# Kernel tuning notes

Hardware: AMD Instinct MI355X
Metric: run time of the kernel (lower is better)

## Reference

```python
import jax, jax.numpy as jnp
import numpy as np

# static config (matches init_kwargs)
P = 16          # proj_patch_dim (window size)
F = 128         # fmap_dim
NH = F // P     # windows per side = 8
N = P * P       # tokens per window = 256
H = 8           # attn_heads
A = 32          # attn_dim (head dim)
C = 32          # leff_filters_out (channels)
INNER = 128     # leff_filters
B = 8           # batch
EPS = 1e-5

# relative-position index (static)
_c = np.stack(np.meshgrid(np.arange(P), np.arange(P), indexing='ij'))  # [2,P,P]
_f = _c.reshape(2, -1)                                                  # [2,N]
_r = _f[:, :, None] - _f[:, None, :]                                    # [2,N,N]
_rpi = (_r[0] + P - 1) * (2 * P - 1) + (_r[1] + P - 1)                  # [N,N]
RPI = jnp.asarray(_rpi.reshape(-1))

# shifted-window attention mask (static)
_sm = np.zeros((F, F), np.float32)
_cnt = 0
_slices = (slice(0, -P), slice(-P, -P // 2), slice(-P // 2, None))
for _hs in _slices:
    for _ws in _slices:
        _sm[_hs, _ws] = _cnt
        _cnt += 1
_smw = _sm.reshape(NH, P, NH, P).transpose(0, 2, 1, 3).reshape(NH * NH, N)
_am = _smw[:, None, :] - _smw[:, :, None]
_am = np.where(_am != 0, np.float32(-100.0), np.float32(0.0))
SHIFT_MASK = jnp.asarray(_am.reshape(1, NH * NH, 1, N, N))


def _ln(x, g, b):
    m = jnp.mean(x, axis=-1, keepdims=True)
    v = jnp.var(x, axis=-1, keepdims=True)
    return (x - m) / jnp.sqrt(v + EPS) * g + b


def setup_inputs() -> dict:
    key = jax.random.key(0)
    ks = jax.random.split(key, 16)
    s = 0.02
    return {
        'x': jax.random.normal(ks[0], (B, F * F, C), jnp.float32),
        'norm1_g': jnp.ones((C,), jnp.float32),
        'norm1_b': jnp.zeros((C,), jnp.float32),
        'mod_w': jax.random.normal(ks[1], (N, C), jnp.float32) * s,
        'qkv_w': jax.random.normal(ks[2], (C, 3 * H * A), jnp.float32) * s,
        'qkv_b': jnp.zeros((3 * H * A,), jnp.float32),
        'rpbt': jax.random.normal(ks[3], ((2 * P - 1) ** 2, H), jnp.float32) * s,
        'rev_w': jax.random.normal(ks[4], (H * A, C), jnp.float32) * s,
        'rev_b': jnp.zeros((C,), jnp.float32),
        'norm2_g': jnp.ones((C,), jnp.float32),
        'norm2_b': jnp.zeros((C,), jnp.float32),
        'lp1_w': jax.random.normal(ks[5], (C, INNER), jnp.float32) * s,
        'lp1_b': jnp.zeros((INNER,), jnp.float32),
        'conv_w': jax.random.normal(ks[6], (3, 3, INNER, INNER), jnp.float32) * s,  # HWIO
        'conv_b': jnp.zeros((INNER,), jnp.float32),
        'lp2_w': jax.random.normal(ks[7], (INNER, C), jnp.float32) * s,
        'lp2_b': jnp.zeros((C,), jnp.float32),
    }


def reference(x, norm1_g, norm1_b, mod_w, qkv_w, qkv_b, rpbt, rev_w, rev_b,
              norm2_g, norm2_b, lp1_w, lp1_b, conv_w, conv_b, lp2_w, lp2_b):
    shortcut = x
    h = _ln(x, norm1_g, norm1_b)
    h = h.reshape(B, F, F, C)
    h = jnp.roll(h, (-P // 2, -P // 2), axis=(1, 2))          # cyclic shift
    # window partition: [B*NH*NH, N, C]
    h = h.reshape(B, NH, P, NH, P, C).transpose(0, 1, 3, 2, 4, 5).reshape(B * NH * NH, N, C)
    h = h + mod_w                                              # learned modulator
    qkv = h @ qkv_w + qkv_b                                    # [W, N, 3*H*A]
    qkv = qkv.reshape(-1, N, 3, H, A).transpose(2, 0, 3, 1, 4) # [3, W, H, N, A]
    q = qkv[0] * (A ** -0.5)
    k = qkv[1]
    v = qkv[2]
    attn = jnp.einsum('whna,whma->whnm', q, k)                 # [W, H, N, N]
    rpb = rpbt[RPI].reshape(N, N, H).transpose(2, 0, 1)        # [H, N, N]
    attn = attn + rpb[None]
    attn = attn.reshape(B, NH * NH, H, N, N) + SHIFT_MASK
    attn = attn.reshape(-1, H, N, N)
    attn = jax.nn.softmax(attn, axis=-1)
    o = jnp.einsum('whnm,whma->whna', attn, v)                 # [W, H, N, A]
    o = o.transpose(0, 2, 1, 3).reshape(-1, N, H * A)
    o = o @ rev_w + rev_b                                      # [W, N, C]
    # window reverse + reverse cyclic shift
    o = o.reshape(B, NH, NH, P, P, C).transpose(0, 1, 3, 2, 4, 5).reshape(B, F, F, C)
    o = jnp.roll(o, (P // 2, P // 2), axis=(1, 2)).reshape(B, F * F, C)
    x_res = shortcut + o
    # LeFF
    y = _ln(x_res, norm2_g, norm2_b)
    y = jax.nn.gelu(y @ lp1_w + lp1_b, approximate=False)
    y = y.reshape(B, F, F, INNER)
    y = jax.lax.conv_general_dilated(y, conv_w, (1, 1), 'SAME',
                                     dimension_numbers=('NHWC', 'HWIO', 'NHWC')) + conv_b
    y = jax.nn.gelu(y, approximate=False)
    y = y.reshape(B, F * F, INNER)
    y = jax.nn.gelu(y @ lp2_w + lp2_b, approximate=False)
    return y + x_res
```

## Files before the change

kernel.cpp:

```cpp
#include <hip/hip_runtime.h>
#include <math.h>

#define Fdim 128
#define Pw   16
#define Hh   8
#define Cc   32
#define Bb   8

typedef short  short8  __attribute__((ext_vector_type(8)));
typedef float  floatx4 __attribute__((ext_vector_type(4)));

#define QSCL   0.2550348637f
#define MASKC2 (-144.26950408889634f)

__device__ __forceinline__ float gelu_f(float x){
    return 0.5f * x * (1.0f + erff(x * 0.70710678118654752f));
}
__device__ __forceinline__ unsigned pk2(float a, float b){
    unsigned ua = (__builtin_bit_cast(unsigned, a) + 0x8000u) >> 16;
    unsigned ub = (__builtin_bit_cast(unsigned, b) + 0x8000u) & 0xffff0000u;
    return ua | ub;
}
__device__ __forceinline__ short bf16s(float a){
    return (short)((__builtin_bit_cast(unsigned, a) + 0x8000u) >> 16);
}
__device__ __forceinline__ float hi2f(unsigned d){ return __builtin_bit_cast(float, d & 0xffff0000u); }
__device__ __forceinline__ float lo2f(unsigned d){ return __builtin_bit_cast(float, d << 16); }

__global__ __launch_bounds__(256) void prep_kernel(
    const float* __restrict__ qkv_w, const float* __restrict__ rev_w,
    const float* __restrict__ rpbt,  const float* __restrict__ lp1_w,
    const float* __restrict__ conv_w, const float* __restrict__ lp2_w,
    short* __restrict__ qkv_wT, short* __restrict__ rev_wT, unsigned* __restrict__ rplb,
    short* __restrict__ lp1_wT, short* __restrict__ conv_wT, short* __restrict__ lp2_wT)
{
    int i = blockIdx.x * 256 + threadIdx.x;
    if (i < 24576){
        int col = i >> 5, c = i & 31;
        qkv_wT[i] = bf16s(qkv_w[c*768 + col]);
    } else if (i < 32768){
        int j = i - 24576;
        int h = j >> 10, r = j & 1023;
        int c = r >> 5, a = r & 31;
        rev_wT[j] = bf16s(rev_w[(h*32 + a)*32 + c]);
    } else if (i < 40464){
        int j = i - 32768;
        int h = j / 962, d = j % 962;
        int g0 = (d < 481) ? (2*d) : (2*(d-481) + 1);
        float f0 = (g0     < 961) ? rpbt[g0*8 + h]*1.4426950408889634f : 0.f;
        float f1 = (g0 + 1 < 961) ? rpbt[(g0+1)*8 + h]*1.4426950408889634f : 0.f;
        rplb[j] = pk2(f0, f1);
    } else if (i < 44560){
        int j = i - 40464;
        int f = j >> 5, c = j & 31;
        lp1_wT[j] = bf16s(lp1_w[c*128 + f]);
    } else if (i < 192016){
        int j = i - 44560;
        int ci_in = j & 7;
        int co    = (j >> 3) & 127;
        int chk   = (j >> 10) & 3;
        int s     = j >> 12;
        int tap = s % 9, kc = s / 9;
        conv_wT[j] = bf16s(conv_w[(tap*128 + kc*32 + chk*8 + ci_in)*128 + co]);
    } else if (i < 196112){
        int j = i - 192016;
        int oc = j >> 7, co = j & 127;
        lp2_wT[j] = bf16s(lp2_w[co*32 + oc]);
    }
}

__global__ __launch_bounds__(512, 4) void attn_kernel(
    const float* __restrict__ x,   const float* __restrict__ n1g,
    const float* __restrict__ n1b, const float* __restrict__ mod_w,
    const float* __restrict__ qkv_b, const float* __restrict__ rev_b,
    const short* __restrict__ qkv_wT, const short* __restrict__ rev_wT,
    const unsigned* __restrict__ rplb,
    float* __restrict__ x_res)
{
    __shared__ __align__(16) short hmodS[4*256*8];
    __shared__ __align__(16) short Kbuf[256*40];
    __shared__ __align__(16) short Qbuf[256*40];
    __shared__ __align__(16) short VTb[32*264];
    __shared__ __align__(16) unsigned rplbS[962];
    __shared__ unsigned regnp[64];

    const int w  = blockIdx.x;
    const int b  = w >> 6;
    const int wi = w & 63;
    const int wh = wi >> 3, ww = wi & 7;
    const int tid  = threadIdx.x;
    const int wv   = tid >> 6;
    const int ln   = tid & 63;
    const int quad = ln >> 4;
    const int l15  = ln & 15;
    const bool masked = (wh == 7) || (ww == 7);

    if (tid < 256){
        const int n  = tid;
        const int rn = n >> 4, cn = n & 15;
        const int gh = (wh*Pw + rn + 8) & 127;
        const int gw = (ww*Pw + cn + 8) & 127;
        const float* xr = x + (((size_t)b << 14) + (gh << 7) + gw) * Cc;
        float v[Cc];
        const float4* x4 = reinterpret_cast<const float4*>(xr);
        float4* v4 = reinterpret_cast<float4*>(v);
        #pragma unroll
        for (int i = 0; i < Cc/4; i++) v4[i] = x4[i];
        float mean = 0.f;
        #pragma unroll
        for (int c = 0; c < Cc; c++) mean += v[c];
        mean *= (1.0f/Cc);
        float var = 0.f;
        #pragma unroll
        for (int c = 0; c < Cc; c++){ float d = v[c] - mean; var = fmaf(d, d, var); }
        var *= (1.0f/Cc);
        const float rinv = rsqrtf(var + 1e-5f);
        #pragma unroll
        for (int c = 0; c < Cc; c++)
            v[c] = (v[c] - mean)*rinv*n1g[c] + n1b[c] + mod_w[n*Cc + c];
        #pragma unroll
        for (int i = 0; i < 4; i++){
            uint4 dw;
            dw.x = pk2(v[8*i+0], v[8*i+1]);
            dw.y = pk2(v[8*i+2], v[8*i+3]);
            dw.z = pk2(v[8*i+4], v[8*i+5]);
            dw.w = pk2(v[8*i+6], v[8*i+7]);
            *(uint4*)(&hmodS[i*2048 + n*8]) = dw;
        }
    }
    if (tid < 64){
        int rm  = tid >> 2;
        int shm = wh*Pw + rm;
        int hreg = (shm < 112) ? 0 : ((shm < 120) ? 1 : 2);
        unsigned dw = 0;
        #pragma unroll
        for (int i = 0; i < 4; i++){
            int cm  = (tid & 3)*4 + i;
            int swm = ww*Pw + cm;
            int wreg = (swm < 112) ? 0 : ((swm < 120) ? 1 : 2);
            dw |= (unsigned)(hreg*3 + wreg) << (8*i);
        }
        regnp[tid] = dw;
    }
    __syncthreads();

    unsigned regq[2] = {0,0};
    if (masked){
        #pragma unroll
        for (int nt = 0; nt < 2; nt++){
            int q = wv*32 + nt*16 + l15;
            regq[nt] = (regnp[q >> 2] >> ((q & 3)*8)) & 255u;
        }
    }

    floatx4 RV[2][2];
    #pragma unroll
    for (int cm = 0; cm < 2; cm++)
        #pragma unroll
        for (int nt = 0; nt < 2; nt++)
            RV[cm][nt] = (floatx4){0.f,0.f,0.f,0.f};

    const int s0lane = 12 + l15 - 4*quad;
    const floatx4 zz = (floatx4){0.f,0.f,0.f,0.f};

    for (int h = 0; h < Hh; h++){
        __syncthreads();

        #pragma unroll
        for (int k2 = 0; k2 < 2; k2++){
            int i = k2*512 + tid;
            if (i < 962) rplbS[i] = rplb[h*962 + i];
        }

        short8 HA[2];
        #pragma unroll
        for (int ii = 0; ii < 2; ii++)
            HA[ii] = *(const short8*)(&hmodS[quad*2048 + (wv*32 + ii*16 + l15)*8]);
        short8 WB[3][2]; float bias[3][2];
        #pragma unroll
        for (int m = 0; m < 3; m++)
            #pragma unroll
            for (int nt = 0; nt < 2; nt++){
                int col = m*256 + h*32 + nt*16 + l15;
                WB[m][nt]  = *(const short8*)(qkv_wT + col*32 + quad*8);
                bias[m][nt] = qkv_b[col];
            }
        #pragma unroll
        for (int ii = 0; ii < 2; ii++){
            int tokbase = wv*32 + ii*16 + quad*4;
            #pragma unroll
            for (int nt = 0; nt < 2; nt++){
                int col = nt*16 + l15;
                floatx4 qf = __builtin_amdgcn_mfma_f32_16x16x32_bf16(HA[ii], WB[0][nt], zz, 0,0,0);
                floatx4 kf = __builtin_amdgcn_mfma_f32_16x16x32_bf16(HA[ii], WB[1][nt], zz, 0,0,0);
                floatx4 vf = __builtin_amdgcn_mfma_f32_16x16x32_bf16(HA[ii], WB[2][nt], zz, 0,0,0);
                float bq = bias[0][nt], bk = bias[1][nt], bv = bias[2][nt];
                #pragma unroll
                for (int r = 0; r < 4; r++){
                    Qbuf[(tokbase + r)*40 + col] = bf16s((qf[r] + bq)*QSCL);
                    Kbuf[(tokbase + r)*40 + col] = bf16s(kf[r] + bk);
                }
                uint2 vv;
                vv.x = pk2(vf[0] + bv, vf[1] + bv);
                vv.y = pk2(vf[2] + bv, vf[3] + bv);
                *(uint2*)(&VTb[col*264 + tokbase]) = vv;
            }
        }
        __syncthreads();

        short8 QB[2];
        #pragma unroll
        for (int nt = 0; nt < 2; nt++)
            QB[nt] = *(const short8*)(&Qbuf[(wv*32 + nt*16 + l15)*40 + quad*8]);

        floatx4 OT[2][2];
        #pragma unroll
        for (int am = 0; am < 2; am++)
            #pragma unroll
            for (int nt = 0; nt < 2; nt++)
                OT[am][nt] = (floatx4){0.f,0.f,0.f,0.f};
        float rs[2] = {0.f,0.f};

        for (int ch = 0; ch < 8; ch++){
            short8 KA[2];
            KA[0] = *(const short8*)(&Kbuf[(ch*32 +      l15)*40 + quad*8]);
            KA[1] = *(const short8*)(&Kbuf[(ch*32 + 16 + l15)*40 + quad*8]);

            unsigned pd0[3], pd1[3];
            int base = wv*2 - ch*2;
            #pragma unroll
            for (int j = 0; j < 3; j++){
                int dt  = base + j - 1;
                int g0  = (dt + 15)*31 + s0lane;
                int dwi = (g0 & 1) ? (481 + (g0 >> 1)) : (g0 >> 1);
                pd0[j] = rplbS[dwi];
                pd1[j] = rplbS[dwi + 1];
            }
            unsigned rk[2] = {0,0};
            if (masked){
                rk[0] = regnp[ch*8 +     quad];
                rk[1] = regnp[ch*8 + 4 + quad];
            }

            floatx4 S[2][2];
            #pragma unroll
            for (int sub = 0; sub < 2; sub++)
                #pragma unroll
                for (int nt = 0; nt < 2; nt++)
                    S[sub][nt] = __builtin_amdgcn_mfma_f32_16x16x32_bf16(KA[sub], QB[nt], zz, 0,0,0);

            #pragma unroll
            for (int sub = 0; sub < 2; sub++)
                #pragma unroll
                for (int nt = 0; nt < 2; nt++){
                    int j = nt - sub + 1;
                    float e0 = S[sub][nt][0] + hi2f(pd1[j]);
                    float e1 = S[sub][nt][1] + lo2f(pd1[j]);
                    float e2 = S[sub][nt][2] + hi2f(pd0[j]);
                    float e3 = S[sub][nt][3] + lo2f(pd0[j]);
                    if (masked){
                        e0 += (((rk[sub]      ) & 255u) == regq[nt]) ? 0.f : MASKC2;
                        e1 += (((rk[sub] >>  8) & 255u) == regq[nt]) ? 0.f : MASKC2;
                        e2 += (((rk[sub] >> 16) & 255u) == regq[nt]) ? 0.f : MASKC2;
                        e3 += (((rk[sub] >> 24) & 255u) == regq[nt]) ? 0.f : MASKC2;
                    }
                    float p0 = exp2f(e0), p1 = exp2f(e1);
                    float p2 = exp2f(e2), p3 = exp2f(e3);
                    rs[nt] += (p0 + p1) + (p2 + p3);
                    uint2 pv; pv.x = pk2(p0, p1); pv.y = pk2(p2, p3);
                    *(uint2*)(&Qbuf[(wv*32 + nt*16 + l15)*40 + sub*16 + quad*4]) = pv;
                }

            short8 VA0 = *(const short8*)(&VTb[(     l15)*264 + ch*32 + quad*8]);
            short8 VA1 = *(const short8*)(&VTb[(16 + l15)*264 + ch*32 + quad*8]);
            #pragma unroll
            for (int nt = 0; nt < 2; nt++){
                short8 PB = *(const short8*)(&Qbuf[(wv*32 + nt*16 + l15)*40 + quad*8]);
                OT[0][nt] = __builtin_amdgcn_mfma_f32_16x16x32_bf16(VA0, PB, OT[0][nt], 0,0,0);
                OT[1][nt] = __builtin_amdgcn_mfma_f32_16x16x32_bf16(VA1, PB, OT[1][nt], 0,0,0);
            }
        }

        float inv[2];
        #pragma unroll
        for (int nt = 0; nt < 2; nt++){
            float t = rs[nt] + __shfl_xor(rs[nt], 16, 64);
            t = t + __shfl_xor(t, 32, 64);
            inv[nt] = 1.0f / t;
        }
        #pragma unroll
        for (int am = 0; am < 2; am++)
            #pragma unroll
            for (int nt = 0; nt < 2; nt++){
                floatx4 o = OT[am][nt];
                float iv = inv[nt];
                uint2 ov;
                ov.x = pk2(o[0]*iv, o[1]*iv);
                ov.y = pk2(o[2]*iv, o[3]*iv);
                *(uint2*)(&Qbuf[(wv*32 + nt*16 + l15)*40 + am*16 + quad*4]) = ov;
            }

        short8 RA0 = *(const short8*)(rev_wT + h*1024 + (     l15)*32 + quad*8);
        short8 RA1 = *(const short8*)(rev_wT + h*1024 + (16 + l15)*32 + quad*8);
        #pragma unroll
        for (int nt = 0; nt < 2; nt++){
            short8 OB = *(const short8*)(&Qbuf[(wv*32 + nt*16 + l15)*40 + quad*8]);
            RV[0][nt] = __builtin_amdgcn_mfma_f32_16x16x32_bf16(RA0, OB, RV[0][nt], 0,0,0);
            RV[1][nt] = __builtin_amdgcn_mfma_f32_16x16x32_bf16(RA1, OB, RV[1][nt], 0,0,0);
        }
    }

    #pragma unroll
    for (int cm = 0; cm < 2; cm++){
        float4 rb = *(const float4*)(rev_b + cm*16 + quad*4);
        #pragma unroll
        for (int nt = 0; nt < 2; nt++){
            int gh = (wh*Pw + wv*2 + nt + 8) & 127;
            int gw = (ww*Pw + l15 + 8) & 127;
            size_t gaddr = (((size_t)b << 14) + (gh << 7) + gw)*Cc + cm*16 + quad*4;
            float4 xv = *(const float4*)(x + gaddr);
            floatx4 o = RV[cm][nt];
            float4 ov;
            ov.x = xv.x + rb.x + o[0];
            ov.y = xv.y + rb.y + o[1];
            ov.z = xv.z + rb.z + o[2];
            ov.w = xv.w + rb.w + o[3];
            *(float4*)(x_res + gaddr) = ov;
        }
    }
}

__global__ __launch_bounds__(512, 4) void leff_kernel(
    const float* __restrict__ x_res, const float* __restrict__ n2g,
    const float* __restrict__ n2b,  const float* __restrict__ lp1_b,
    const float* __restrict__ conv_b, const float* __restrict__ lp2_b,
    const short* __restrict__ lp1_wT, const short* __restrict__ conv_wT,
    const short* __restrict__ lp2_wT, float* __restrict__ out)
{
    __shared__ __align__(16) char lds[70144];
    short* xa   = (short*)lds;
    short* y1c  = (short*)(lds + 26880);
    short* wbuf = (short*)(lds + 53760);
    short* y2   = (short*)lds;

    const int blk = blockIdx.x;
    const int b   = blk >> 6;
    const int ty  = (blk >> 3) & 7, tx = blk & 7;
    const int tid  = threadIdx.x;
    const int wv   = tid >> 6;
    const int ln   = tid & 63;
    const int quad = ln >> 4;
    const int l15  = ln & 15;
    const floatx4 zz = (floatx4){0.f,0.f,0.f,0.f};

    if (tid < 336){
        int hp = tid;
        int hy = hp / 18, hx = hp - hy*18;
        int gy = ty*16 + hy - 1, gx = tx*16 + hx - 1;
        bool ok = (hp < 324) && ((unsigned)gy < 128u) && ((unsigned)gx < 128u);
        if (ok){
            const float* xr = x_res + (((size_t)b << 14) + (gy << 7) + gx)*Cc;
            float v[Cc];
            const float4* x4 = reinterpret_cast<const float4*>(xr);
            float4* v4 = reinterpret_cast<float4*>(v);
            #pragma unroll
            for (int i = 0; i < Cc/4; i++) v4[i] = x4[i];
            float mean = 0.f;
            #pragma unroll
            for (int c = 0; c < Cc; c++) mean += v[c];
            mean *= (1.0f/Cc);
            float var = 0.f;
            #pragma unroll
            for (int c = 0; c < Cc; c++){ float d = v[c] - mean; var = fmaf(d, d, var); }
            var *= (1.0f/Cc);
            const float rinv = rsqrtf(var + 1e-5f);
            #pragma unroll
            for (int i = 0; i < 4; i++){
                float w0 = (v[8*i+0]-mean)*rinv*n2g[8*i+0] + n2b[8*i+0];
                float w1 = (v[8*i+1]-mean)*rinv*n2g[8*i+1] + n2b[8*i+1];
                float w2 = (v[8*i+2]-mean)*rinv*n2g[8*i+2] + n2b[8*i+2];
                float w3 = (v[8*i+3]-mean)*rinv*n2g[8*i+3] + n2b[8*i+3];
                float w4 = (v[8*i+4]-mean)*rinv*n2g[8*i+4] + n2b[8*i+4];
                float w5 = (v[8*i+5]-mean)*rinv*n2g[8*i+5] + n2b[8*i+5];
                float w6 = (v[8*i+6]-mean)*rinv*n2g[8*i+6] + n2b[8*i+6];
                float w7 = (v[8*i+7]-mean)*rinv*n2g[8*i+7] + n2b[8*i+7];
                uint4 dw;
                dw.x = pk2(w0,w1); dw.y = pk2(w2,w3);
                dw.z = pk2(w4,w5); dw.w = pk2(w6,w7);
                *(uint4*)(xa + hp*40 + i*8) = dw;
            }
        } else {
            uint4 z = {0,0,0,0};
            #pragma unroll
            for (int i = 0; i < 4; i++) *(uint4*)(xa + hp*40 + i*8) = z;
        }
    }

    ((uint4*)wbuf)[tid] = ((const uint4*)conv_wT)[tid];

    floatx4 acc[2][8];
    #pragma unroll
    for (int j = 0; j < 2; j++)
        #pragma unroll
        for (int m = 0; m < 8; m++) acc[j][m] = zz;

    for (int idx = 0; idx < 36; idx++){
        const int kc  = idx / 9;
        const int tap = idx - kc*9;

        if (tap == 0){
            __syncthreads();
            short8 A1[2]; float4 b1[2];
            #pragma unroll
            for (int mt = 0; mt < 2; mt++){
                A1[mt] = *(const short8*)(lp1_wT + (kc*32 + mt*16 + l15)*32 + quad*8);
                b1[mt] = *(const float4*)(lp1_b + kc*32 + mt*16 + quad*4);
            }
            #pragma unroll
            for (int ii = 0; ii < 3; ii++){
                int nt = wv + 8*ii;
                if (nt < 21){
                    int px = nt*16 + l15;
                    int hy = px / 18, hx = px - hy*18;
                    int gy = ty*16 + hy - 1, gx = tx*16 + hx - 1;
                    bool oob = (px >= 324) || ((unsigned)gy > 127u) || ((unsigned)gx > 127u);
                    short8 Bx = *(const short8*)(xa + px*40 + quad*8);
                    #pragma unroll
                    for (int mt = 0; mt < 2; mt++){
                        floatx4 c = __builtin_amdgcn_mfma_f32_16x16x32_bf16(A1[mt], Bx, zz, 0,0,0);
                        float v0 = oob ? 0.f : gelu_f(c[0] + b1[mt].x);
                        float v1 = oob ? 0.f : gelu_f(c[1] + b1[mt].y);
                        float v2 = oob ? 0.f : gelu_f(c[2] + b1[mt].z);
                        float v3 = oob ? 0.f : gelu_f(c[3] + b1[mt].w);
                        uint2 pv; pv.x = pk2(v0, v1); pv.y = pk2(v2, v3);
                        *(uint2*)(y1c + px*40 + mt*16 + quad*4) = pv;
                    }
                }
            }
        }

        uint4 pf;
        if (idx < 35) pf = ((const uint4*)conv_wT)[(idx + 1)*512 + tid];

        __syncthreads();

        const short* wb = wbuf + (idx & 1)*4096;
        const int ky = tap / 3, kx = tap - ky*3;

        short8 Bf[2];
        #pragma unroll
        for (int j = 0; j < 2; j++){
            int oy = wv*2 + j;
            int hp = (oy + ky)*18 + kx + l15;
            Bf[j] = *(const short8*)(y1c + hp*40 + quad*8);
        }
        #pragma unroll
        for (int m = 0; m < 8; m++){
            short8 Aw = *(const short8*)(wb + quad*1024 + (m*16 + l15)*8);
            acc[0][m] = __builtin_amdgcn_mfma_f32_16x16x32_bf16(Aw, Bf[0], acc[0][m], 0,0,0);
            acc[1][m] = __builtin_amdgcn_mfma_f32_16x16x32_bf16(Aw, Bf[1], acc[1][m], 0,0,0);
        }

        if (idx < 35)
            ((uint4*)(wbuf + ((idx + 1) & 1)*4096))[tid] = pf;
    }

    __syncthreads();

    #pragma unroll
    for (int j = 0; j < 2; j++){
        int px = (wv*2 + j)*16 + l15;
        #pragma unroll
        for (int m = 0; m < 8; m++){
            float4 cb = *(const float4*)(conv_b + m*16 + quad*4);
            floatx4 a = acc[j][m];
            float v0 = gelu_f(a[0] + cb.x);
            float v1 = gelu_f(a[1] + cb.y);
            float v2 = gelu_f(a[2] + cb.z);
            float v3 = gelu_f(a[3] + cb.w);
            uint2 pv; pv.x = pk2(v0, v1); pv.y = pk2(v2, v3);
            *(uint2*)(y2 + px*136 + m*16 + quad*4) = pv;
        }
    }
    __syncthreads();

    short8 A2[2][4]; float4 lb[2];
    #pragma unroll
    for (int mt = 0; mt < 2; mt++){
        #pragma unroll
        for (int k = 0; k < 4; k++)
            A2[mt][k] = *(const short8*)(lp2_wT + (mt*16 + l15)*128 + k*32 + quad*8);
        lb[mt] = *(const float4*)(lp2_b + mt*16 + quad*4);
    }
    #pragma unroll
    for (int j = 0; j < 2; j++){
        int oy = wv*2 + j;
        floatx4 c2[2] = {zz, zz};
        #pragma unroll
        for (int k = 0; k < 4; k++){
            short8 Bf = *(const short8*)(y2 + (oy*16 + l15)*136 + k*32 + quad*8);
            c2[0] = __builtin_amdgcn_mfma_f32_16x16x32_bf16(A2[0][k], Bf, c2[0], 0,0,0);
            c2[1] = __builtin_amdgcn_mfma_f32_16x16x32_bf16(A2[1][k], Bf, c2[1], 0,0,0);
        }
        int gy = ty*16 + oy, gx = tx*16 + l15;
        size_t base = (((size_t)b << 14) + (gy << 7) + gx)*Cc;
        #pragma unroll
        for (int mt = 0; mt < 2; mt++){
            size_t ad = base + mt*16 + quad*4;
            float4 xr = *(const float4*)(x_res + ad);
            float4 ov;
            ov.x = gelu_f(c2[mt][0] + lb[mt].x) + xr.x;
            ov.y = gelu_f(c2[mt][1] + lb[mt].y) + xr.y;
            ov.z = gelu_f(c2[mt][2] + lb[mt].z) + xr.z;
            ov.w = gelu_f(c2[mt][3] + lb[mt].w) + xr.w;
            *(float4*)(out + ad) = ov;
        }
    }
}

extern "C" void kernel_launch(void* const* d_in, const int* in_sizes, int n_in,
                              void* d_out, int out_size, void* d_ws, size_t ws_size,
                              hipStream_t stream)
{
    (void)in_sizes; (void)n_in; (void)out_size; (void)ws_size;
    const float* x      = (const float*)d_in[0];
    const float* n1g    = (const float*)d_in[1];
    const float* n1b    = (const float*)d_in[2];
    const float* mod_w  = (const float*)d_in[3];
    const float* qkv_w  = (const float*)d_in[4];
    const float* qkv_b  = (const float*)d_in[5];
    const float* rpbt   = (const float*)d_in[6];
    const float* rev_w  = (const float*)d_in[7];
    const float* rev_b  = (const float*)d_in[8];
    const float* n2g    = (const float*)d_in[9];
    const float* n2b    = (const float*)d_in[10];
    const float* lp1_w  = (const float*)d_in[11];
    const float* lp1_b  = (const float*)d_in[12];
    const float* conv_w = (const float*)d_in[13];
    const float* conv_b = (const float*)d_in[14];
    const float* lp2_w  = (const float*)d_in[15];
    const float* lp2_b  = (const float*)d_in[16];
    float* out = (float*)d_out;

    char* wsb = (char*)d_ws;
    float*    x_res  = (float*)wsb;
    short*    qkv_wT = (short*)(wsb + 16777216);
    short*    rev_wT = (short*)(wsb + 16826368);
    unsigned* rplbT  = (unsigned*)(wsb + 16842752);
    short*    lp1_wT = (short*)(wsb + 16873536);
    short*    conv_wT= (short*)(wsb + 16881728);
    short*    lp2_wT = (short*)(wsb + 17176640);

    prep_kernel<<<767, 256, 0, stream>>>(qkv_w, rev_w, rpbt, lp1_w, conv_w, lp2_w,
                                         qkv_wT, rev_wT, rplbT, lp1_wT, conv_wT, lp2_wT);
    attn_kernel<<<512, 512, 0, stream>>>(x, n1g, n1b, mod_w, qkv_b, rev_b,
                                         qkv_wT, rev_wT, rplbT, x_res);
    leff_kernel<<<512, 512, 0, stream>>>(x_res, n2g, n2b, lp1_b, conv_b, lp2_b,
                                         lp1_wT, conv_wT, lp2_wT, out);
}
```

Measured before the change: 289.7 us.

## Move softmax row sums, bias adds and QKV transposes into MFMA operations

The change pre-loads the relative-position bias and shift mask into the MFMA accumulator so the score MFMA performs the bias add. It computes softmax row sums with an extra MFMA against a ones vector instead of scalar adds plus cross-lane shuffles. Q and K are computed transposed so each lane writes packed 8-byte stores instead of scalar 2-byte stores. bf16 packing now uses a single byte-permute instruction. The aim is fewer VALU, shuffle and LDS store instructions. The cost is extra MFMA work, and the row sums now come from bf16-rounded probabilities.

```diff
diff --git a/kernel.cpp b/kernel.cpp
--- a/kernel.cpp
+++ b/kernel.cpp
@@ -17,9 +17,9 @@
     return 0.5f * x * (1.0f + erff(x * 0.70710678118654752f));
 }
 __device__ __forceinline__ unsigned pk2(float a, float b){
-    unsigned ua = (__builtin_bit_cast(unsigned, a) + 0x8000u) >> 16;
-    unsigned ub = (__builtin_bit_cast(unsigned, b) + 0x8000u) & 0xffff0000u;
-    return ua | ub;
+    unsigned ua = __builtin_bit_cast(unsigned, a) + 0x8000u;
+    unsigned ub = __builtin_bit_cast(unsigned, b) + 0x8000u;
+    return __builtin_amdgcn_perm(ub, ua, 0x07060302);
 }
 __device__ __forceinline__ short bf16s(float a){
     return (short)((__builtin_bit_cast(unsigned, a) + 0x8000u) >> 16);
@@ -162,6 +162,7 @@
 
     const int s0lane = 12 + l15 - 4*quad;
     const floatx4 zz = (floatx4){0.f,0.f,0.f,0.f};
+    const short8 ONEv = {0x3F80,0x3F80,0x3F80,0x3F80,0x3F80,0x3F80,0x3F80,0x3F80};
 
     for (int h = 0; h < Hh; h++){
         __syncthreads();
@@ -172,38 +173,41 @@
             if (i < 962) rplbS[i] = rplb[h*962 + i];
         }
 
-        short8 HA[2];
+        short8 HF[2];
         #pragma unroll
         for (int ii = 0; ii < 2; ii++)
-            HA[ii] = *(const short8*)(&hmodS[quad*2048 + (wv*32 + ii*16 + l15)*8]);
-        short8 WB[3][2]; float bias[3][2];
-        #pragma unroll
-        for (int m = 0; m < 3; m++)
-            #pragma unroll
-            for (int nt = 0; nt < 2; nt++){
-                int col = m*256 + h*32 + nt*16 + l15;
-                WB[m][nt]  = *(const short8*)(qkv_wT + col*32 + quad*8);
-                bias[m][nt] = qkv_b[col];
-            }
+            HF[ii] = *(const short8*)(&hmodS[quad*2048 + (wv*32 + ii*16 + l15)*8]);
+        short8 WQ[2], WK[2], WVb[2];
+        float4 bq[2], bk[2]; float bv[2];
+        #pragma unroll
+        for (int mt = 0; mt < 2; mt++){
+            WQ[mt]  = *(const short8*)(qkv_wT + (      h*32 + mt*16 + l15)*32 + quad*8);
+            WK[mt]  = *(const short8*)(qkv_wT + (256 + h*32 + mt*16 + l15)*32 + quad*8);
+            WVb[mt] = *(const short8*)(qkv_wT + (512 + h*32 + mt*16 + l15)*32 + quad*8);
+            bq[mt]  = *(const float4*)(qkv_b +       h*32 + mt*16 + quad*4);
+            bk[mt]  = *(const float4*)(qkv_b + 256 + h*32 + mt*16 + quad*4);
+            bv[mt]  = qkv_b[512 + h*32 + mt*16 + l15];
+        }
         #pragma unroll
         for (int ii = 0; ii < 2; ii++){
-            int tokbase = wv*32 + ii*16 + quad*4;
-            #pragma unroll
-            for (int nt = 0; nt < 2; nt++){
-                int col = nt*16 + l15;
-                floatx4 qf = __builtin_amdgcn_mfma_f32_16x16x32_bf16(HA[ii], WB[0][nt], zz, 0,0,0);
-                floatx4 kf = __builtin_amdgcn_mfma_f32_16x16x32_bf16(HA[ii], WB[1][nt], zz, 0,0,0);
-                floatx4 vf = __builtin_amdgcn_mfma_f32_16x16x32_bf16(HA[ii], WB[2][nt], zz, 0,0,0);
-                float bq = bias[0][nt], bk = bias[1][nt], bv = bias[2][nt];
-                #pragma unroll
-                for (int r = 0; r < 4; r++){
-                    Qbuf[(tokbase + r)*40 + col] = bf16s((qf[r] + bq)*QSCL);
-                    Kbuf[(tokbase + r)*40 + col] = bf16s(kf[r] + bk);
-                }
+            const int tok = wv*32 + ii*16;
+            #pragma unroll
+            for (int mt = 0; mt < 2; mt++){
+                floatx4 qf = __builtin_amdgcn_mfma_f32_16x16x32_bf16(WQ[mt], HF[ii], zz, 0,0,0);
+                floatx4 kf = __builtin_amdgcn_mfma_f32_16x16x32_bf16(WK[mt], HF[ii], zz, 0,0,0);
+                floatx4 vf = __builtin_amdgcn_mfma_f32_16x16x32_bf16(HF[ii], WVb[mt], zz, 0,0,0);
+                uint2 qv;
+                qv.x = pk2((qf[0]+bq[mt].x)*QSCL, (qf[1]+bq[mt].y)*QSCL);
+                qv.y = pk2((qf[2]+bq[mt].z)*QSCL, (qf[3]+bq[mt].w)*QSCL);
+                *(uint2*)(&Qbuf[(tok + l15)*40 + mt*16 + quad*4]) = qv;
+                uint2 kv;
+                kv.x = pk2(kf[0]+bk[mt].x, kf[1]+bk[mt].y);
+                kv.y = pk2(kf[2]+bk[mt].z, kf[3]+bk[mt].w);
+                *(uint2*)(&Kbuf[(tok + l15)*40 + mt*16 + quad*4]) = kv;
                 uint2 vv;
-                vv.x = pk2(vf[0] + bv, vf[1] + bv);
-                vv.y = pk2(vf[2] + bv, vf[3] + bv);
-                *(uint2*)(&VTb[col*264 + tokbase]) = vv;
+                vv.x = pk2(vf[0]+bv[mt], vf[1]+bv[mt]);
+                vv.y = pk2(vf[2]+bv[mt], vf[3]+bv[mt]);
+                *(uint2*)(&VTb[(mt*16 + l15)*264 + tok + quad*4]) = vv;
             }
         }
         __syncthreads();
@@ -219,7 +223,7 @@
             #pragma unroll
             for (int nt = 0; nt < 2; nt++)
                 OT[am][nt] = (floatx4){0.f,0.f,0.f,0.f};
-        float rs[2] = {0.f,0.f};
+        floatx4 RS[2] = {zz, zz};
 
         for (int ch = 0; ch < 8; ch++){
             short8 KA[2];
@@ -242,34 +246,27 @@
                 rk[1] = regnp[ch*8 + 4 + quad];
             }
 
-            floatx4 S[2][2];
-            #pragma unroll
-            for (int sub = 0; sub < 2; sub++)
-                #pragma unroll
-                for (int nt = 0; nt < 2; nt++)
-                    S[sub][nt] = __builtin_amdgcn_mfma_f32_16x16x32_bf16(KA[sub], QB[nt], zz, 0,0,0);
-
-            #pragma unroll
-            for (int sub = 0; sub < 2; sub++)
+            #pragma unroll
+            for (int sub = 0; sub < 2; sub++){
                 #pragma unroll
                 for (int nt = 0; nt < 2; nt++){
                     int j = nt - sub + 1;
-                    float e0 = S[sub][nt][0] + hi2f(pd1[j]);
-                    float e1 = S[sub][nt][1] + lo2f(pd1[j]);
-                    float e2 = S[sub][nt][2] + hi2f(pd0[j]);
-                    float e3 = S[sub][nt][3] + lo2f(pd0[j]);
+                    floatx4 ci;
+                    ci[0] = hi2f(pd1[j]); ci[1] = lo2f(pd1[j]);
+                    ci[2] = hi2f(pd0[j]); ci[3] = lo2f(pd0[j]);
                     if (masked){
-                        e0 += (((rk[sub]      ) & 255u) == regq[nt]) ? 0.f : MASKC2;
-                        e1 += (((rk[sub] >>  8) & 255u) == regq[nt]) ? 0.f : MASKC2;
-                        e2 += (((rk[sub] >> 16) & 255u) == regq[nt]) ? 0.f : MASKC2;
-                        e3 += (((rk[sub] >> 24) & 255u) == regq[nt]) ? 0.f : MASKC2;
+                        ci[0] += (((rk[sub]      ) & 255u) == regq[nt]) ? 0.f : MASKC2;
+                        ci[1] += (((rk[sub] >>  8) & 255u) == regq[nt]) ? 0.f : MASKC2;
+                        ci[2] += (((rk[sub] >> 16) & 255u) == regq[nt]) ? 0.f : MASKC2;
+                        ci[3] += (((rk[sub] >> 24) & 255u) == regq[nt]) ? 0.f : MASKC2;
                     }
-                    float p0 = exp2f(e0), p1 = exp2f(e1);
-                    float p2 = exp2f(e2), p3 = exp2f(e3);
-                    rs[nt] += (p0 + p1) + (p2 + p3);
+                    floatx4 S = __builtin_amdgcn_mfma_f32_16x16x32_bf16(KA[sub], QB[nt], ci, 0,0,0);
+                    float p0 = exp2f(S[0]), p1 = exp2f(S[1]);
+                    float p2 = exp2f(S[2]), p3 = exp2f(S[3]);
                     uint2 pv; pv.x = pk2(p0, p1); pv.y = pk2(p2, p3);
                     *(uint2*)(&Qbuf[(wv*32 + nt*16 + l15)*40 + sub*16 + quad*4]) = pv;
                 }
+            }
 
             short8 VA0 = *(const short8*)(&VTb[(     l15)*264 + ch*32 + quad*8]);
             short8 VA1 = *(const short8*)(&VTb[(16 + l15)*264 + ch*32 + quad*8]);
@@ -278,16 +275,13 @@
                 short8 PB = *(const short8*)(&Qbuf[(wv*32 + nt*16 + l15)*40 + quad*8]);
                 OT[0][nt] = __builtin_amdgcn_mfma_f32_16x16x32_bf16(VA0, PB, OT[0][nt], 0,0,0);
                 OT[1][nt] = __builtin_amdgcn_mfma_f32_16x16x32_bf16(VA1, PB, OT[1][nt], 0,0,0);
+                RS[nt]    = __builtin_amdgcn_mfma_f32_16x16x32_bf16(ONEv, PB, RS[nt], 0,0,0);
             }
         }
 
         float inv[2];
-        #pragma unroll
-        for (int nt = 0; nt < 2; nt++){
-            float t = rs[nt] + __shfl_xor(rs[nt], 16, 64);
-            t = t + __shfl_xor(t, 32, 64);
-            inv[nt] = 1.0f / t;
-        }
+        inv[0] = 1.0f / RS[0][0];
+        inv[1] = 1.0f / RS[1][0];
         #pragma unroll
         for (int am = 0; am < 2; am++)
             #pragma unroll
```

Result: faster. 276.6 us (-4.5%).
